# Kernel tuning notes

Hardware: AMD Instinct MI355X
Metric: run time of the kernel (lower is better)

## Reference

```python
import jax, jax.numpy as jnp
import numpy as np

ALPHA = 0.2  # leaky relu slope


def _gat(h, W, b, a_src, a_dst, a_b):
    # h: [B,T,Din]; W: [H,Din,C]; b,a_src,a_dst: [H,C]; a_b: [H]
    Wh = jnp.einsum('btd,hdc->bhtc', h, W) + b[None, :, None, :]
    src = jnp.einsum('bhtc,hc->bht', Wh, a_src)  # score from Wh_i half of concat
    dst = jnp.einsum('bhtc,hc->bht', Wh, a_dst)  # score from Wh_j half
    e = src[:, :, :, None] + dst[:, :, None, :] + a_b[None, :, None, None]  # [B,H,T,T]
    e = jnp.where(e >= 0, e, ALPHA * e)  # leaky_relu
    a = jax.nn.softmax(e, axis=-1)
    out = jnp.einsum('bhij,bhjc->bhic', a, Wh)
    out = jax.nn.relu(out)  # last=False branch
    B, H, T, C = out.shape
    out = out.transpose(0, 2, 1, 3).reshape(B, T, H * C)  # concat heads on feature dim
    return jax.nn.sigmoid(out)


def setup_inputs() -> dict:
    key = jax.random.key(0)
    ks = jax.random.split(key, 15)
    B, T, D = 16, 128, 256
    H, C1, C2, OUT_W = 64, 64, 20, 32
    s = lambda k, shape, fan: jax.random.normal(k, shape, jnp.float32) * (1.0 / np.sqrt(fan))
    return {
        'x': jax.random.normal(ks[0], (B, T, D), jnp.float32),
        'W1': s(ks[1], (H, D, C1), D), 'b1': s(ks[2], (H, C1), D),
        'a1s': s(ks[3], (H, C1), 2 * C1), 'a1d': s(ks[4], (H, C1), 2 * C1),
        'a1b': s(ks[5], (H,), 2 * C1),
        'W2': s(ks[6], (H, H * C1, C2), H * C1), 'b2': s(ks[7], (H, C2), H * C1),
        'a2s': s(ks[8], (H, C2), 2 * C2), 'a2d': s(ks[9], (H, C2), 2 * C2),
        'a2b': s(ks[10], (H,), 2 * C2),
        'sl_w': s(ks[11], (H * C2, D), H * C2), 'sl_b': s(ks[12], (D,), H * C2),
        'gar_w': s(ks[13], (T, OUT_W), T), 'gar_b': s(ks[14], (OUT_W,), T),
    }


def reference(x, W1, b1, a1s, a1d, a1b, W2, b2, a2s, a2d, a2b, sl_w, sl_b, gar_w, gar_b):
    c = _gat(x, W1, b1, a1s, a1d, a1b)          # [B,T,H*C1]
    c = jax.nn.relu(c)
    c = _gat(c, W2, b2, a2s, a2d, a2b)          # [B,T,H*C2]
    c = c @ sl_w + sl_b                          # [B,T,D]
    # GAR: linear over time dim: [B,T,D] -> [B,OUT_W,D]
    res = jnp.einsum('btd,to->bod', c, gar_w) + gar_b[None, :, None]
    return res
```

## Files before the change

### kernel.cpp

```cpp
#include <hip/hip_runtime.h>
#include <hip/hip_bf16.h>

#define B 16
#define T 128
#define D 256
#define H 64
#define C1 64
#define C2 20
#define K2 4096
#define F2 1280
#define OUTW 32
#define ALPHA 0.2f

typedef __attribute__((ext_vector_type(8))) short short8;
typedef __attribute__((ext_vector_type(4))) float f32x4;

static __device__ __forceinline__ ushort f2bf(float f) {
    __hip_bfloat16 h = __float2bfloat16(f);
    return *reinterpret_cast<ushort*>(&h);
}
static __device__ __forceinline__ float bf2f(ushort u) {
    return __uint_as_float(((unsigned int)u) << 16);
}
static __device__ __forceinline__ void gload16(const ushort* g, ushort* l) {
    __builtin_amdgcn_global_load_lds((const unsigned int*)g, (unsigned int*)l,
                                     16, 0, 0);
}

template<int KD, int NBLK, int MBLK, int KSPLIT, int PERM>
__global__ __launch_bounds__(256) void gemm_splitk_kernel(
    const ushort* __restrict__ Ag, const ushort* __restrict__ Bg,
    ushort* __restrict__ Cp)
{
    __shared__ ushort As[128 * 64];
    __shared__ ushort Bs[128 * 64];
    constexpr int NN = NBLK * 128;
    constexpr int MM = MBLK * 128;
    constexpr int NT = MBLK * NBLK;
    constexpr int TOTAL = NT * KSPLIT;
    constexpr int KDP = KD / KSPLIT;
    static_assert(TOTAL % 8 == 0, "swizzle needs multiple of 8 blocks");

    int tid = threadIdx.x;
    int bid = blockIdx.x;
    int wg = (bid & 7) * (TOTAL / 8) + (bid >> 3);
    int kp = wg / NT; int tile = wg - kp * NT;
    int bm = (tile / NBLK) * 128, bn = (tile % NBLK) * 128;

    int wave = tid >> 6, lane = tid & 63;
    int wm = (wave >> 1) * 64, wn = (wave & 1) * 64;
    int lr = lane & 15, lk = lane >> 4;
    int srow = lane >> 3, scol = (lane & 7) * 8;

    f32x4 acc[4][4];
    #pragma unroll
    for (int i = 0; i < 4; ++i)
        #pragma unroll
        for (int j = 0; j < 4; ++j) acc[i][j] = (f32x4){0.f, 0.f, 0.f, 0.f};

    const ushort* ApB = Ag + (size_t)bm * KD + kp * KDP;
    const ushort* BpB = Bg + (size_t)bn * KD + kp * KDP;

    for (int k0 = 0; k0 < KDP; k0 += 64) {
        __syncthreads();
        #pragma unroll
        for (int e = 0; e < 4; ++e) {
            int c = e * 4 + wave;
            gload16(ApB + (size_t)(8 * c + srow) * KD + k0 + scol, &As[c * 512]);
            gload16(BpB + (size_t)(8 * c + srow) * KD + k0 + scol, &Bs[c * 512]);
        }
        __syncthreads();
        #pragma unroll
        for (int ks = 0; ks < 2; ++ks) {
            short8 af[4], bfr[4];
            #pragma unroll
            for (int i = 0; i < 4; ++i)
                af[i] = *(const short8*)&As[(wm + i * 16 + lr) * 64 + ks * 32 + lk * 8];
            #pragma unroll
            for (int j = 0; j < 4; ++j)
                bfr[j] = *(const short8*)&Bs[(wn + j * 16 + lr) * 64 + ks * 32 + lk * 8];
            #pragma unroll
            for (int i = 0; i < 4; ++i)
                #pragma unroll
                for (int j = 0; j < 4; ++j)
                    acc[i][j] = __builtin_amdgcn_mfma_f32_16x16x32_bf16(
                        af[i], bfr[j], acc[i][j], 0, 0, 0);
        }
    }

    if constexpr (PERM) {
        ushort* Cw = Cp + (size_t)kp * MM * NN + (size_t)tile * 16384
                   + wave * 4096 + lane * 4;
        #pragma unroll
        for (int i = 0; i < 4; ++i)
            #pragma unroll
            for (int j = 0; j < 4; ++j) {
                union { ushort q[4]; uint2 v; } pk;
                #pragma unroll
                for (int r = 0; r < 4; ++r) pk.q[r] = f2bf(acc[i][j][r]);
                *(uint2*)&Cw[(i * 4 + j) * 256] = pk.v;
            }
    } else {
        ushort* Cout = Cp + (size_t)kp * MM * NN;
        #pragma unroll
        for (int i = 0; i < 4; ++i) {
            #pragma unroll
            for (int j = 0; j < 4; ++j) {
                int col = bn + wn + j * 16 + lr;
                #pragma unroll
                for (int r = 0; r < 4; ++r) {
                    int row = bm + wm + i * 16 + lk * 4 + r;
                    Cout[(size_t)row * NN + col] = f2bf(acc[i][j][r]);
                }
            }
        }
    }
}

template<int P, int NN>
__global__ __launch_bounds__(256) void reduce_bias_kernel(
    const ushort* __restrict__ parts, const float* __restrict__ bias,
    float* __restrict__ out, int MN)
{
    size_t off = ((size_t)blockIdx.x * 256 + threadIdx.x) * 4;
    float s0 = 0.f, s1 = 0.f, s2 = 0.f, s3 = 0.f;
    #pragma unroll
    for (int p = 0; p < P; ++p) {
        uint2 v = *(const uint2*)&parts[(size_t)p * MN + off];
        s0 += bf2f((ushort)(v.x & 0xffff));
        s1 += bf2f((ushort)(v.x >> 16));
        s2 += bf2f((ushort)(v.y & 0xffff));
        s3 += bf2f((ushort)(v.y >> 16));
    }
    float4 bv = *(const float4*)&bias[(int)(off % NN)];
    float4 o; o.x = s0 + bv.x; o.y = s1 + bv.y; o.z = s2 + bv.z; o.w = s3 + bv.w;
    *(float4*)&out[off] = o;
}

#define AS_(r,c)  u.stag[(r) * 72 + (c)]
#define BS_(r,c)  u.stag[9216 + (r) * 72 + (c)]
#define PB_(r,c)  u.Pb[(r) * 136 + (c)]
#define WHT_(r,c) whT[(r) * 136 + (c)]

__global__ __launch_bounds__(256) void fused1_kernel(
    const ushort* __restrict__ xbf,
    const ushort* __restrict__ w1t,
    const float* __restrict__ b1,
    const float* __restrict__ a1s, const float* __restrict__ a1d,
    const float* __restrict__ a1b,
    ushort* __restrict__ c1)
{
    int blk = blockIdx.x; int b = blk >> 6, h = blk & 63;
    __shared__ union {
        ushort stag[128 * 72 + 64 * 72];
        ushort Pb[128 * 136];
    } u;
    __shared__ ushort whT[64 * 136];
    __shared__ float ss[128], ddv[128], sinv[128];

    int tid = threadIdx.x;
    int wave = tid >> 6, lane = tid & 63;
    int wm = (wave >> 1) * 64, wn = (wave & 1) * 32;
    int lr = lane & 15, lk = lane >> 4;
    int sr = tid >> 3, sc = (tid & 7) * 8;

    f32x4 acc[4][2];
    #pragma unroll
    for (int i = 0; i < 4; ++i)
        #pragma unroll
        for (int j = 0; j < 2; ++j) acc[i][j] = (f32x4){0.f, 0.f, 0.f, 0.f};

    const ushort* Ap = xbf + (size_t)(b * T + sr) * D + sc;
    const ushort* Bp = w1t + (size_t)(h * 64 + sr) * D + sc;

    uint4 ra[4], rb[2];
    #pragma unroll
    for (int e = 0; e < 4; ++e) ra[e] = *(const uint4*)(Ap + (size_t)e * 32 * D);
    #pragma unroll
    for (int e = 0; e < 2; ++e) rb[e] = *(const uint4*)(Bp + (size_t)e * 32 * D);

    for (int k0 = 0; k0 < D; k0 += 64) {
        __syncthreads();
        #pragma unroll
        for (int e = 0; e < 4; ++e) *(uint4*)&AS_(sr + e * 32, sc) = ra[e];
        if (sr < 32) {
            #pragma unroll
            for (int e = 0; e < 2; ++e) *(uint4*)&BS_(sr + e * 32, sc) = rb[e];
        }
        __syncthreads();
        if (k0 + 64 < D) {
            #pragma unroll
            for (int e = 0; e < 4; ++e)
                ra[e] = *(const uint4*)(Ap + (size_t)e * 32 * D + k0 + 64);
            #pragma unroll
            for (int e = 0; e < 2; ++e)
                rb[e] = *(const uint4*)(Bp + (size_t)e * 32 * D + k0 + 64);
        }
        #pragma unroll
        for (int ks = 0; ks < 2; ++ks) {
            short8 af[4], bfr[2];
            #pragma unroll
            for (int i = 0; i < 4; ++i)
                af[i] = *(const short8*)&AS_(wm + i * 16 + lr, ks * 32 + lk * 8);
            #pragma unroll
            for (int j = 0; j < 2; ++j)
                bfr[j] = *(const short8*)&BS_(wn + j * 16 + lr, ks * 32 + lk * 8);
            #pragma unroll
            for (int i = 0; i < 4; ++i)
                #pragma unroll
                for (int j = 0; j < 2; ++j)
                    acc[i][j] = __builtin_amdgcn_mfma_f32_16x16x32_bf16(
                        af[i], bfr[j], acc[i][j], 0, 0, 0);
        }
    }

    #pragma unroll
    for (int j = 0; j < 2; ++j) {
        int col = wn + j * 16 + lr;
        float bv = b1[h * C1 + col];
        #pragma unroll
        for (int i = 0; i < 4; ++i) {
            int t0 = wm + i * 16 + lk * 4;
            union { ushort q[4]; uint2 v; } pk;
            #pragma unroll
            for (int r = 0; r < 4; ++r) pk.q[r] = f2bf(acc[i][j][r] + bv);
            *(uint2*)&WHT_(col, t0) = pk.v;
        }
    }
    __syncthreads();

    {
        int t = tid & 127;
        bool isS = tid < 128;
        const float* av = (isS ? a1s : a1d) + h * C1;
        float s = isS ? a1b[h] : 0.f;
        #pragma unroll 8
        for (int c = 0; c < 64; ++c) s = fmaf(bf2f(WHT_(c, t)), av[c], s);
        if (isS) ss[t] = s; else ddv[t] = s;
    }
    __syncthreads();

    {
        float dm = fmaxf(ddv[lane], ddv[lane + 64]);
        #pragma unroll
        for (int msk = 1; msk < 64; msk <<= 1) dm = fmaxf(dm, __shfl_xor(dm, msk));
        int i = tid >> 1, j0 = (tid & 1) * 64;
        float si = ss[i];
        float mx = si + dm; mx = mx >= 0.f ? mx : ALPHA * mx;
        float lsum = 0.f;
        #pragma unroll
        for (int g = 0; g < 8; ++g) {
            union { ushort q[8]; uint4 v; } pk;
            #pragma unroll
            for (int e = 0; e < 8; ++e) {
                float ee = si + ddv[j0 + g * 8 + e];
                ee = ee >= 0.f ? ee : ALPHA * ee;
                float pp = __expf(ee - mx);
                lsum += pp;
                pk.q[e] = f2bf(pp);
            }
            *(uint4*)&PB_(i, j0 + g * 8) = pk.v;
        }
        lsum += __shfl_xor(lsum, 1);
        if (!(tid & 1)) sinv[i] = 1.0f / lsum;
    }
    __syncthreads();

    f32x4 acc2[4][2];
    #pragma unroll
    for (int i = 0; i < 4; ++i)
        #pragma unroll
        for (int j = 0; j < 2; ++j) acc2[i][j] = (f32x4){0.f, 0.f, 0.f, 0.f};

    #pragma unroll
    for (int ks = 0; ks < 4; ++ks) {
        short8 af[4], bfr[2];
        #pragma unroll
        for (int i = 0; i < 4; ++i)
            af[i] = *(const short8*)&PB_(wm + i * 16 + lr, ks * 32 + lk * 8);
        #pragma unroll
        for (int j = 0; j < 2; ++j)
            bfr[j] = *(const short8*)&WHT_(wn + j * 16 + lr, ks * 32 + lk * 8);
        #pragma unroll
        for (int i = 0; i < 4; ++i)
            #pragma unroll
            for (int j = 0; j < 2; ++j)
                acc2[i][j] = __builtin_amdgcn_mfma_f32_16x16x32_bf16(
                    af[i], bfr[j], acc2[i][j], 0, 0, 0);
    }

    __syncthreads();
    ushort* CT = u.Pb;
    #pragma unroll
    for (int i = 0; i < 4; ++i) {
        #pragma unroll
        for (int r = 0; r < 4; ++r) {
            int row = wm + i * 16 + lk * 4 + r;
            float sv = sinv[row];
            #pragma unroll
            for (int j = 0; j < 2; ++j) {
                int col = wn + j * 16 + lr;
                float v = acc2[i][j][r] * sv;
                v = v > 0.f ? v : 0.f;
                v = 1.0f / (1.0f + __expf(-v));
                CT[row * 72 + col] = f2bf(v);
            }
        }
    }
    __syncthreads();
    #pragma unroll
    for (int e = 0; e < 4; ++e) {
        int idx = e * 256 + tid;
        int row = idx >> 3, q = idx & 7;
        uint4 v = *(const uint4*)&CT[row * 72 + q * 8];
        *(uint4*)&c1[((size_t)(b * T + row)) * K2 + h * C1 + q * 8] = v;
    }
}

#define PB2_(r,c)  Pb2[(r) * 136 + (c)]
#define WHT2_(r,c) whT2[(r) * 136 + (c)]

__global__ __launch_bounds__(256) void fused2_kernel(
    const ushort* __restrict__ wh2pb,
    const float* __restrict__ b2,
    const float* __restrict__ a2s, const float* __restrict__ a2d,
    const float* __restrict__ a2b,
    ushort* __restrict__ c2)
{
    int blk = blockIdx.x; int b = blk >> 6, h = blk & 63;
    __shared__ ushort Pb2[128 * 136];
    __shared__ ushort whT2[32 * 136];
    __shared__ float ss[128], ddv[128], sinv[128];

    int tid = threadIdx.x;
    int wave = tid >> 6, lane = tid & 63;
    int lr = lane & 15, lk = lane >> 4;
    const size_t MNfull = (size_t)2048 * F2;

    for (int e = 0; e < 10; ++e) {
        int idx = e * 256 + tid;
        int t = idx / 20, c = idx - t * 20;
        int col = h * C2 + c;
        int tn = col >> 7, cl = col & 127;
        int wv = ((t >> 6) << 1) | (cl >> 6);
        int fi = (t >> 4) & 3, fk = (t >> 2) & 3, fr = t & 3;
        int fj = (cl >> 4) & 3, fl = cl & 15;
        size_t fa = (size_t)(b * 10 + tn) * 16384 + wv * 4096
                  + (fi * 4 + fj) * 256 + (fk * 16 + fl) * 4 + fr;
        float s = b2[col];
        #pragma unroll
        for (int p = 0; p < 8; ++p) s += bf2f(wh2pb[p * MNfull + fa]);
        WHT2_(c, t) = f2bf(s);
    }
    {
        int idx = tid;
        for (int e = 0; e < 6; ++e, idx += 256) {
            int c = 20 + (idx >> 7), t = idx & 127;
            WHT2_(c, t) = 0;
        }
    }
    __syncthreads();

    {
        int t = tid & 127;
        bool isS = tid < 128;
        const float* av = (isS ? a2s : a2d) + h * C2;
        float s = isS ? a2b[h] : 0.f;
        #pragma unroll
        for (int c = 0; c < 20; ++c) s = fmaf(bf2f(WHT2_(c, t)), av[c], s);
        if (isS) ss[t] = s; else ddv[t] = s;
    }
    __syncthreads();

    {
        float dm = fmaxf(ddv[lane], ddv[lane + 64]);
        #pragma unroll
        for (int msk = 1; msk < 64; msk <<= 1) dm = fmaxf(dm, __shfl_xor(dm, msk));
        int i = tid >> 1, j0 = (tid & 1) * 64;
        float si = ss[i];
        float mx = si + dm; mx = mx >= 0.f ? mx : ALPHA * mx;
        float lsum = 0.f;
        #pragma unroll
        for (int g = 0; g < 8; ++g) {
            union { ushort q[8]; uint4 v; } pk;
            #pragma unroll
            for (int e = 0; e < 8; ++e) {
                float ee = si + ddv[j0 + g * 8 + e];
                ee = ee >= 0.f ? ee : ALPHA * ee;
                float pp = __expf(ee - mx);
                lsum += pp;
                pk.q[e] = f2bf(pp);
            }
            *(uint4*)&PB2_(i, j0 + g * 8) = pk.v;
        }
        lsum += __shfl_xor(lsum, 1);
        if (!(tid & 1)) sinv[i] = 1.0f / lsum;
    }
    __syncthreads();

    int wm2 = wave * 32;
    f32x4 acc2[2][2];
    #pragma unroll
    for (int i = 0; i < 2; ++i)
        #pragma unroll
        for (int j = 0; j < 2; ++j) acc2[i][j] = (f32x4){0.f, 0.f, 0.f, 0.f};

    #pragma unroll
    for (int ks = 0; ks < 4; ++ks) {
        short8 af[2], bfr[2];
        #pragma unroll
        for (int i = 0; i < 2; ++i)
            af[i] = *(const short8*)&PB2_(wm2 + i * 16 + lr, ks * 32 + lk * 8);
        #pragma unroll
        for (int j = 0; j < 2; ++j)
            bfr[j] = *(const short8*)&WHT2_(j * 16 + lr, ks * 32 + lk * 8);
        #pragma unroll
        for (int i = 0; i < 2; ++i)
            #pragma unroll
            for (int j = 0; j < 2; ++j)
                acc2[i][j] = __builtin_amdgcn_mfma_f32_16x16x32_bf16(
                    af[i], bfr[j], acc2[i][j], 0, 0, 0);
    }

    __syncthreads();
    ushort* CT2 = Pb2;
    #pragma unroll
    for (int i = 0; i < 2; ++i) {
        #pragma unroll
        for (int r = 0; r < 4; ++r) {
            int row = wm2 + i * 16 + lk * 4 + r;
            float sv = sinv[row];
            #pragma unroll
            for (int j = 0; j < 2; ++j) {
                int col = j * 16 + lr;
                if (col < C2) {
                    float v = acc2[i][j][r] * sv;
                    v = v > 0.f ? v : 0.f;
                    v = 1.0f / (1.0f + __expf(-v));
                    CT2[row * 24 + col] = f2bf(v);
                }
            }
        }
    }
    __syncthreads();
    for (int e = 0; e < 3; ++e) {
        int idx = e * 256 + tid;
        if (idx < 640) {
            int row = idx / 5, q = idx - row * 5;
            uint2 v = *(const uint2*)&CT2[row * 24 + q * 4];
            *(uint2*)&c2[((size_t)(b * T + row)) * F2 + h * C2 + q * 4] = v;
        }
    }
}

__global__ __launch_bounds__(256) void xbf_kernel(
    const float* __restrict__ x, ushort* __restrict__ xbf)
{
    int i = blockIdx.x * 256 + threadIdx.x;
    float4 v = *(const float4*)&x[(size_t)i * 4];
    union { ushort u[4]; uint2 p; } o;
    o.u[0] = f2bf(v.x); o.u[1] = f2bf(v.y);
    o.u[2] = f2bf(v.z); o.u[3] = f2bf(v.w);
    *(uint2*)&xbf[(size_t)i * 4] = o.p;
}

__global__ __launch_bounds__(256) void w1t_kernel(
    const float* __restrict__ W1, ushort* __restrict__ w1t)
{
    int blk = blockIdx.x; int h = blk >> 2, d0 = (blk & 3) * 64;
    __shared__ float lw[64][65];
    int tid = threadIdx.x;
    for (int e = 0; e < 16; ++e) {
        int idx = e * 256 + tid; int dr = idx >> 6, c = idx & 63;
        lw[dr][c] = W1[((size_t)h * D + d0 + dr) * C1 + c];
    }
    __syncthreads();
    for (int e = 0; e < 16; ++e) {
        int idx = e * 256 + tid; int c = idx >> 6, dr = idx & 63;
        w1t[((size_t)(h * 64 + c)) * D + d0 + dr] = f2bf(lw[dr][c]);
    }
}

__global__ __launch_bounds__(256) void w2t_kernel(
    const float* __restrict__ W2, ushort* __restrict__ w2t)
{
    int blk = blockIdx.x; int h = blk >> 5, kb = blk & 31; int k0 = kb * 128;
    __shared__ float lw[128][21];
    int tid = threadIdx.x;
    const float* src = W2 + ((size_t)h * K2 + k0) * C2;
    for (int e = 0; e < 10; ++e) {
        int idx = e * 256 + tid; int k = idx / 20, c = idx - k * 20;
        lw[k][c] = src[idx];
    }
    __syncthreads();
    for (int e = 0; e < 10; ++e) {
        int idx = e * 256 + tid; int c = idx >> 7, k = idx & 127;
        w2t[((size_t)(h * 20 + c)) * K2 + k0 + k] = f2bf(lw[k][c]);
    }
}

__global__ __launch_bounds__(256) void slwt_kernel(
    const float* __restrict__ slw, ushort* __restrict__ slwt)
{
    int blk = blockIdx.x; int kb = blk >> 2, d0 = (blk & 3) * 64; int k0 = kb * 64;
    __shared__ float lw[64][65];
    int tid = threadIdx.x;
    for (int e = 0; e < 16; ++e) {
        int idx = e * 256 + tid; int kr = idx >> 6, dc = idx & 63;
        lw[kr][dc] = slw[((size_t)(k0 + kr)) * D + d0 + dc];
    }
    __syncthreads();
    for (int e = 0; e < 16; ++e) {
        int idx = e * 256 + tid; int dr = idx >> 6, kc = idx & 63;
        slwt[((size_t)(d0 + dr)) * F2 + k0 + kc] = f2bf(lw[kc][dr]);
    }
}

__global__ __launch_bounds__(256) void gar_kernel(
    const float* __restrict__ c3, const float* __restrict__ garw,
    const float* __restrict__ garb, float* __restrict__ out)
{
    int blk = blockIdx.x; int b = blk >> 5, o = blk & 31;
    int dcol = threadIdx.x;
    float acc = garb[o];
    const float* cp = c3 + (size_t)b * T * D + dcol;
    for (int t = 0; t < T; ++t)
        acc = fmaf(cp[(size_t)t * D], garw[t * OUTW + o], acc);
    out[((size_t)b * OUTW + o) * D + dcol] = acc;
}

extern "C" void kernel_launch(void* const* d_in, const int* in_sizes, int n_in,
                              void* d_out, int out_size, void* d_ws, size_t ws_size,
                              hipStream_t stream) {
    const float* x    = (const float*)d_in[0];
    const float* W1   = (const float*)d_in[1];
    const float* b1   = (const float*)d_in[2];
    const float* a1s  = (const float*)d_in[3];
    const float* a1d  = (const float*)d_in[4];
    const float* a1b  = (const float*)d_in[5];
    const float* W2   = (const float*)d_in[6];
    const float* b2   = (const float*)d_in[7];
    const float* a2s  = (const float*)d_in[8];
    const float* a2d  = (const float*)d_in[9];
    const float* a2b  = (const float*)d_in[10];
    const float* slw  = (const float*)d_in[11];
    const float* slb  = (const float*)d_in[12];
    const float* garw = (const float*)d_in[13];
    const float* garb = (const float*)d_in[14];

    char* p = (char*)d_ws;
    float*  c3    = (float*)p;   p += (size_t)2048 * 256  * 4;
    ushort* xbf   = (ushort*)p;  p += (size_t)2048 * 256  * 2;
    ushort* w1t   = (ushort*)p;  p += (size_t)4096 * 256  * 2;
    ushort* c1bf  = (ushort*)p;  p += (size_t)2048 * 4096 * 2;
    ushort* w2t   = (ushort*)p;  p += (size_t)1280 * 4096 * 2;
    ushort* c2bf  = (ushort*)p;  p += (size_t)2048 * 1280 * 2;
    ushort* slwt  = (ushort*)p;  p += (size_t)256  * 1280 * 2;
    ushort* wh2pb = (ushort*)p;  p += (size_t)8 * 2048 * 1280 * 2;
    ushort* c3pb  = (ushort*)c1bf;

    xbf_kernel <<<512,  256, 0, stream>>>(x, xbf);
    w1t_kernel <<<256,  256, 0, stream>>>(W1, w1t);
    w2t_kernel <<<2048, 256, 0, stream>>>(W2, w2t);
    slwt_kernel<<<80,   256, 0, stream>>>(slw, slwt);

    fused1_kernel<<<B * H, 256, 0, stream>>>(xbf, w1t, b1, a1s, a1d, a1b, c1bf);

    gemm_splitk_kernel<4096, 10, 16, 8, 1><<<1280, 256, 0, stream>>>(c1bf, w2t,
                                                                     wh2pb);
    fused2_kernel<<<B * H, 256, 0, stream>>>(wh2pb, b2, a2s, a2d, a2b, c2bf);

    gemm_splitk_kernel<1280, 2, 16, 4, 0><<<128, 256, 0, stream>>>(c2bf, slwt,
                                                                   c3pb);
    reduce_bias_kernel<4, 256><<<512, 256, 0, stream>>>(c3pb, slb, c3, 2048 * 256);

    gar_kernel<<<B * OUTW, 256, 0, stream>>>(c3, garw, garb, (float*)d_out);
}
```

Before: 131.6 us.

## Store layer-1 GAT output head-blocked and read it contiguously in second GEMM

fused1 now writes each (batch, head) 128x64 output tile as one contiguous block instead of scattering rows across the 4096-wide concatenated feature dimension. A dedicated gemm2 kernel reads the A operand from this head-blocked layout, so each 64-wide K slice is a contiguous 8 KB chunk. The aim is fully coalesced stores in fused1 and contiguous loads in the split-K GEMM. It adds a specialised GEMM kernel tied to this layout, and the generic GEMM loses its permuted-output option.

```diff
diff --git a/kernel.cpp b/kernel.cpp
--- a/kernel.cpp
+++ b/kernel.cpp
@@ -27,7 +27,85 @@
                                      16, 0, 0);
 }
 
-template<int KD, int NBLK, int MBLK, int KSPLIT, int PERM>
+template<int NBLK, int MBLK, int KSPLIT>
+__global__ __launch_bounds__(256) void gemm2_kernel(
+    const ushort* __restrict__ Ag,
+    const ushort* __restrict__ Bg,
+    ushort* __restrict__ Cp)
+{
+    __shared__ ushort As[128 * 64];
+    __shared__ ushort Bs[128 * 64];
+    constexpr int KD = 4096;
+    constexpr int NN = NBLK * 128;
+    constexpr int MM = MBLK * 128;
+    constexpr int NT = MBLK * NBLK;
+    constexpr int TOTAL = NT * KSPLIT;
+    constexpr int KDP = KD / KSPLIT;
+    static_assert(TOTAL % 8 == 0, "swizzle needs multiple of 8 blocks");
+
+    int tid = threadIdx.x;
+    int bid = blockIdx.x;
+    int wg = (bid & 7) * (TOTAL / 8) + (bid >> 3);
+    int kp = wg / NT; int tile = wg - kp * NT;
+    int bb = tile / NBLK, bn = (tile % NBLK) * 128;
+
+    int wave = tid >> 6, lane = tid & 63;
+    int wm = (wave >> 1) * 64, wn = (wave & 1) * 64;
+    int lr = lane & 15, lk = lane >> 4;
+    int srow = lane >> 3, scol = (lane & 7) * 8;
+
+    f32x4 acc[4][4];
+    #pragma unroll
+    for (int i = 0; i < 4; ++i)
+        #pragma unroll
+        for (int j = 0; j < 4; ++j) acc[i][j] = (f32x4){0.f, 0.f, 0.f, 0.f};
+
+    const ushort* BpB = Bg + (size_t)bn * KD + kp * KDP;
+    const ushort* ApB = Ag + (size_t)(bb * 64 + kp * 8) * 8192;
+
+    for (int k0 = 0; k0 < KDP; k0 += 64) {
+        int hh = k0 >> 6;
+        __syncthreads();
+        #pragma unroll
+        for (int e = 0; e < 4; ++e) {
+            int c = e * 4 + wave;
+            gload16(ApB + (size_t)hh * 8192 + (8 * c + srow) * 64 + scol,
+                    &As[c * 512]);
+            gload16(BpB + (size_t)(8 * c + srow) * KD + k0 + scol, &Bs[c * 512]);
+        }
+        __syncthreads();
+        #pragma unroll
+        for (int ks = 0; ks < 2; ++ks) {
+            short8 af[4], bfr[4];
+            #pragma unroll
+            for (int i = 0; i < 4; ++i)
+                af[i] = *(const short8*)&As[(wm + i * 16 + lr) * 64 + ks * 32 + lk * 8];
+            #pragma unroll
+            for (int j = 0; j < 4; ++j)
+                bfr[j] = *(const short8*)&Bs[(wn + j * 16 + lr) * 64 + ks * 32 + lk * 8];
+            #pragma unroll
+            for (int i = 0; i < 4; ++i)
+                #pragma unroll
+                for (int j = 0; j < 4; ++j)
+                    acc[i][j] = __builtin_amdgcn_mfma_f32_16x16x32_bf16(
+                        af[i], bfr[j], acc[i][j], 0, 0, 0);
+        }
+    }
+
+    ushort* Cw = Cp + (size_t)kp * MM * NN + (size_t)tile * 16384
+               + wave * 4096 + lane * 4;
+    #pragma unroll
+    for (int i = 0; i < 4; ++i)
+        #pragma unroll
+        for (int j = 0; j < 4; ++j) {
+            union { ushort q[4]; uint2 v; } pk;
+            #pragma unroll
+            for (int r = 0; r < 4; ++r) pk.q[r] = f2bf(acc[i][j][r]);
+            *(uint2*)&Cw[(i * 4 + j) * 256] = pk.v;
+        }
+}
+
+template<int KD, int NBLK, int MBLK, int KSPLIT>
 __global__ __launch_bounds__(256) void gemm_splitk_kernel(
     const ushort* __restrict__ Ag, const ushort* __restrict__ Bg,
     ushort* __restrict__ Cp)
@@ -88,30 +166,16 @@
         }
     }
 
-    if constexpr (PERM) {
-        ushort* Cw = Cp + (size_t)kp * MM * NN + (size_t)tile * 16384
-                   + wave * 4096 + lane * 4;
-        #pragma unroll
-        for (int i = 0; i < 4; ++i)
-            #pragma unroll
-            for (int j = 0; j < 4; ++j) {
-                union { ushort q[4]; uint2 v; } pk;
-                #pragma unroll
-                for (int r = 0; r < 4; ++r) pk.q[r] = f2bf(acc[i][j][r]);
-                *(uint2*)&Cw[(i * 4 + j) * 256] = pk.v;
-            }
-    } else {
-        ushort* Cout = Cp + (size_t)kp * MM * NN;
-        #pragma unroll
-        for (int i = 0; i < 4; ++i) {
-            #pragma unroll
-            for (int j = 0; j < 4; ++j) {
-                int col = bn + wn + j * 16 + lr;
-                #pragma unroll
-                for (int r = 0; r < 4; ++r) {
-                    int row = bm + wm + i * 16 + lk * 4 + r;
-                    Cout[(size_t)row * NN + col] = f2bf(acc[i][j][r]);
-                }
+    ushort* Cout = Cp + (size_t)kp * MM * NN;
+    #pragma unroll
+    for (int i = 0; i < 4; ++i) {
+        #pragma unroll
+        for (int j = 0; j < 4; ++j) {
+            int col = bn + wn + j * 16 + lr;
+            #pragma unroll
+            for (int r = 0; r < 4; ++r) {
+                int row = bm + wm + i * 16 + lk * 4 + r;
+                Cout[(size_t)row * NN + col] = f2bf(acc[i][j][r]);
             }
         }
     }
@@ -308,12 +372,13 @@
         }
     }
     __syncthreads();
+    ushort* c1blk = c1 + (size_t)blk * (128 * 64);
     #pragma unroll
     for (int e = 0; e < 4; ++e) {
         int idx = e * 256 + tid;
         int row = idx >> 3, q = idx & 7;
         uint4 v = *(const uint4*)&CT[row * 72 + q * 8];
-        *(uint4*)&c1[((size_t)(b * T + row)) * K2 + h * C1 + q * 8] = v;
+        *(uint4*)&c1blk[row * 64 + q * 8] = v;
     }
 }
 
@@ -566,12 +631,11 @@
 
     fused1_kernel<<<B * H, 256, 0, stream>>>(xbf, w1t, b1, a1s, a1d, a1b, c1bf);
 
-    gemm_splitk_kernel<4096, 10, 16, 8, 1><<<1280, 256, 0, stream>>>(c1bf, w2t,
-                                                                     wh2pb);
+    gemm2_kernel<10, 16, 8><<<1280, 256, 0, stream>>>(c1bf, w2t, wh2pb);
     fused2_kernel<<<B * H, 256, 0, stream>>>(wh2pb, b2, a2s, a2d, a2b, c2bf);
 
-    gemm_splitk_kernel<1280, 2, 16, 4, 0><<<128, 256, 0, stream>>>(c2bf, slwt,
-                                                                   c3pb);
+    gemm_splitk_kernel<1280, 2, 16, 4><<<128, 256, 0, stream>>>(c2bf, slwt,
+                                                                c3pb);
     reduce_bias_kernel<4, 256><<<512, 256, 0, stream>>>(c3pb, slb, c3, 2048 * 256);
 
     gar_kernel<<<B * OUTW, 256, 0, stream>>>(c3, garw, garb, (float*)d_out);
```

Result: slower. 140.9 us (+7.1%).

## Load GEMM fragments directly from global and compute softmax probabilities in registers

Applied to the files above, without the earlier changes.

The first-layer projection GEMM in fused1_kernel now loads MFMA operand fragments straight from global memory instead of staging tiles through LDS. The attention softmax probabilities are computed in registers in MFMA A-fragment layout and fed directly into the P·Wh MFMA, so the LDS P buffer and several barriers go away. Row sums are reduced with cross-lane shuffles. This cuts LDS footprint and synchronization, which may allow more resident blocks, but global fragment loads are less coalesced and each wave's exp work is recomputed per column-half (two waves share rows).

```diff
diff --git a/kernel.cpp b/kernel.cpp
--- a/kernel.cpp
+++ b/kernel.cpp
@@ -137,9 +137,6 @@
     *(float4*)&out[off] = o;
 }
 
-#define AS_(r,c)  u.stag[(r) * 72 + (c)]
-#define BS_(r,c)  u.stag[9216 + (r) * 72 + (c)]
-#define PB_(r,c)  u.Pb[(r) * 136 + (c)]
 #define WHT_(r,c) whT[(r) * 136 + (c)]
 
 __global__ __launch_bounds__(256) void fused1_kernel(
@@ -151,18 +148,14 @@
     ushort* __restrict__ c1)
 {
     int blk = blockIdx.x; int b = blk >> 6, h = blk & 63;
-    __shared__ union {
-        ushort stag[128 * 72 + 64 * 72];
-        ushort Pb[128 * 136];
-    } u;
     __shared__ ushort whT[64 * 136];
+    __shared__ ushort CT[128 * 72];
     __shared__ float ss[128], ddv[128], sinv[128];
 
     int tid = threadIdx.x;
     int wave = tid >> 6, lane = tid & 63;
     int wm = (wave >> 1) * 64, wn = (wave & 1) * 32;
     int lr = lane & 15, lk = lane >> 4;
-    int sr = tid >> 3, sc = (tid & 7) * 8;
 
     f32x4 acc[4][2];
     #pragma unroll
@@ -170,48 +163,24 @@
         #pragma unroll
         for (int j = 0; j < 2; ++j) acc[i][j] = (f32x4){0.f, 0.f, 0.f, 0.f};
 
-    const ushort* Ap = xbf + (size_t)(b * T + sr) * D + sc;
-    const ushort* Bp = w1t + (size_t)(h * 64 + sr) * D + sc;
-
-    uint4 ra[4], rb[2];
-    #pragma unroll
-    for (int e = 0; e < 4; ++e) ra[e] = *(const uint4*)(Ap + (size_t)e * 32 * D);
-    #pragma unroll
-    for (int e = 0; e < 2; ++e) rb[e] = *(const uint4*)(Bp + (size_t)e * 32 * D);
-
-    for (int k0 = 0; k0 < D; k0 += 64) {
-        __syncthreads();
-        #pragma unroll
-        for (int e = 0; e < 4; ++e) *(uint4*)&AS_(sr + e * 32, sc) = ra[e];
-        if (sr < 32) {
-            #pragma unroll
-            for (int e = 0; e < 2; ++e) *(uint4*)&BS_(sr + e * 32, sc) = rb[e];
-        }
-        __syncthreads();
-        if (k0 + 64 < D) {
-            #pragma unroll
-            for (int e = 0; e < 4; ++e)
-                ra[e] = *(const uint4*)(Ap + (size_t)e * 32 * D + k0 + 64);
-            #pragma unroll
-            for (int e = 0; e < 2; ++e)
-                rb[e] = *(const uint4*)(Bp + (size_t)e * 32 * D + k0 + 64);
-        }
-        #pragma unroll
-        for (int ks = 0; ks < 2; ++ks) {
-            short8 af[4], bfr[2];
-            #pragma unroll
-            for (int i = 0; i < 4; ++i)
-                af[i] = *(const short8*)&AS_(wm + i * 16 + lr, ks * 32 + lk * 8);
+    const ushort* Abase = xbf + (size_t)(b * T + wm + lr) * D + lk * 8;
+    const ushort* Bbase = w1t + (size_t)(h * 64 + wn + lr) * D + lk * 8;
+
+    #pragma unroll 2
+    for (int kb = 0; kb < 8; ++kb) {
+        short8 af[4], bfr[2];
+        #pragma unroll
+        for (int i = 0; i < 4; ++i)
+            af[i] = *(const short8*)(Abase + (size_t)i * 16 * D + kb * 32);
+        #pragma unroll
+        for (int j = 0; j < 2; ++j)
+            bfr[j] = *(const short8*)(Bbase + (size_t)j * 16 * D + kb * 32);
+        #pragma unroll
+        for (int i = 0; i < 4; ++i)
             #pragma unroll
             for (int j = 0; j < 2; ++j)
-                bfr[j] = *(const short8*)&BS_(wn + j * 16 + lr, ks * 32 + lk * 8);
-            #pragma unroll
-            for (int i = 0; i < 4; ++i)
-                #pragma unroll
-                for (int j = 0; j < 2; ++j)
-                    acc[i][j] = __builtin_amdgcn_mfma_f32_16x16x32_bf16(
-                        af[i], bfr[j], acc[i][j], 0, 0, 0);
-        }
+                acc[i][j] = __builtin_amdgcn_mfma_f32_16x16x32_bf16(
+                    af[i], bfr[j], acc[i][j], 0, 0, 0);
     }
 
     #pragma unroll
@@ -240,57 +209,63 @@
     }
     __syncthreads();
 
-    {
-        float dm = fmaxf(ddv[lane], ddv[lane + 64]);
-        #pragma unroll
-        for (int msk = 1; msk < 64; msk <<= 1) dm = fmaxf(dm, __shfl_xor(dm, msk));
-        int i = tid >> 1, j0 = (tid & 1) * 64;
-        float si = ss[i];
-        float mx = si + dm; mx = mx >= 0.f ? mx : ALPHA * mx;
-        float lsum = 0.f;
-        #pragma unroll
-        for (int g = 0; g < 8; ++g) {
-            union { ushort q[8]; uint4 v; } pk;
+    float dm = fmaxf(ddv[lane], ddv[lane + 64]);
+    #pragma unroll
+    for (int msk = 1; msk < 64; msk <<= 1) dm = fmaxf(dm, __shfl_xor(dm, msk));
+
+    float si[4], mi[4], rsum[4];
+    #pragma unroll
+    for (int i = 0; i < 4; ++i) {
+        si[i] = ss[wm + i * 16 + lr];
+        float mx = si[i] + dm;
+        mi[i] = mx >= 0.f ? mx : ALPHA * mx;
+        rsum[i] = 0.f;
+    }
+
+    f32x4 acc2[4][2];
+    #pragma unroll
+    for (int i = 0; i < 4; ++i)
+        #pragma unroll
+        for (int j = 0; j < 2; ++j) acc2[i][j] = (f32x4){0.f, 0.f, 0.f, 0.f};
+
+    #pragma unroll
+    for (int ks = 0; ks < 4; ++ks) {
+        float dj[8];
+        #pragma unroll
+        for (int e = 0; e < 8; ++e) dj[e] = ddv[ks * 32 + lk * 8 + e];
+        short8 bfr[2];
+        #pragma unroll
+        for (int j = 0; j < 2; ++j)
+            bfr[j] = *(const short8*)&WHT_(wn + j * 16 + lr, ks * 32 + lk * 8);
+        #pragma unroll
+        for (int i = 0; i < 4; ++i) {
+            union { ushort q[8]; short8 s; } pk;
             #pragma unroll
             for (int e = 0; e < 8; ++e) {
-                float ee = si + ddv[j0 + g * 8 + e];
+                float ee = si[i] + dj[e];
                 ee = ee >= 0.f ? ee : ALPHA * ee;
-                float pp = __expf(ee - mx);
-                lsum += pp;
+                float pp = __expf(ee - mi[i]);
+                rsum[i] += pp;
                 pk.q[e] = f2bf(pp);
             }
-            *(uint4*)&PB_(i, j0 + g * 8) = pk.v;
-        }
-        lsum += __shfl_xor(lsum, 1);
-        if (!(tid & 1)) sinv[i] = 1.0f / lsum;
-    }
-    __syncthreads();
-
-    f32x4 acc2[4][2];
-    #pragma unroll
-    for (int i = 0; i < 4; ++i)
-        #pragma unroll
-        for (int j = 0; j < 2; ++j) acc2[i][j] = (f32x4){0.f, 0.f, 0.f, 0.f};
-
-    #pragma unroll
-    for (int ks = 0; ks < 4; ++ks) {
-        short8 af[4], bfr[2];
-        #pragma unroll
-        for (int i = 0; i < 4; ++i)
-            af[i] = *(const short8*)&PB_(wm + i * 16 + lr, ks * 32 + lk * 8);
-        #pragma unroll
-        for (int j = 0; j < 2; ++j)
-            bfr[j] = *(const short8*)&WHT_(wn + j * 16 + lr, ks * 32 + lk * 8);
-        #pragma unroll
-        for (int i = 0; i < 4; ++i)
             #pragma unroll
             for (int j = 0; j < 2; ++j)
                 acc2[i][j] = __builtin_amdgcn_mfma_f32_16x16x32_bf16(
-                    af[i], bfr[j], acc2[i][j], 0, 0, 0);
-    }
-
-    __syncthreads();
-    ushort* CT = u.Pb;
+                    pk.s, bfr[j], acc2[i][j], 0, 0, 0);
+        }
+    }
+
+    #pragma unroll
+    for (int i = 0; i < 4; ++i) {
+        rsum[i] += __shfl_xor(rsum[i], 16);
+        rsum[i] += __shfl_xor(rsum[i], 32);
+    }
+    if (lk == 0) {
+        #pragma unroll
+        for (int i = 0; i < 4; ++i) sinv[wm + i * 16 + lr] = 1.0f / rsum[i];
+    }
+    __syncthreads();
+
     #pragma unroll
     for (int i = 0; i < 4; ++i) {
         #pragma unroll
```

Result: no change. 133.3 us (+1.3%).
